# Performance work log

Hardware: AMD Instinct MI355X
Metric: run time of the kernel (lower is better)

## Reference

```python
import jax, jax.numpy as jnp
import numpy as np

K = 16          # num neighbor samples
SHARE = 8       # share_planes


def _conv1x1(x, w, b=None):
    # x: [B, Cin, N, K], w: [Cout, Cin]
    y = jnp.einsum('oc,bcnk->bonk', w, x)
    if b is not None:
        y = y + b[None, :, None, None]
    return y


def setup_inputs() -> dict:
    key = jax.random.key(0)
    ks = jax.random.split(key, 18)
    B, CIN, N = 4, 64, 16384
    MID, OUT, PT = 64, 128, 8
    s = 0.05  # weight scale

    def w(k, shape):
        return jax.random.normal(k, shape, jnp.float32) * s

    return {
        'sm_feats': jax.random.normal(ks[0], (B, CIN, N, K), jnp.float32),
        'sm_ppfs': jax.random.normal(ks[1], (B, PT, N, K), jnp.float32),
        'w0': w(ks[2], (OUT, CIN)),   'b0': w(ks[3], (OUT,)),
        'w1': w(ks[4], (MID, OUT)),   'b1': w(ks[5], (MID,)),
        'w2': w(ks[6], (MID, OUT)),   'b2': w(ks[7], (MID,)),
        'w3': w(ks[8], (MID, OUT)),   'b3': w(ks[9], (MID,)),
        'pw1': w(ks[10], (MID, PT)),
        'pw2': w(ks[11], (MID, MID)),
        'cw1': w(ks[12], (MID // SHARE, MID * K)),
        'cw2': w(ks[13], (K * MID // SHARE, MID // SHARE)), 'cb2': w(ks[14], (K * MID // SHARE,)),
        'wout': w(ks[15], (OUT, MID)), 'bout': w(ks[16], (OUT,)),
    }


def reference(sm_feats, sm_ppfs, w0, b0, w1, b1, w2, b2, w3, b3,
              pw1, pw2, cw1, cw2, cb2, wout, bout):
    B, _, N, k = sm_feats.shape
    xn = jax.nn.relu(_conv1x1(sm_feats, w0, b0))          # [B, OUT, N, K]
    x = xn[:, :, :, 0:1]                                   # [B, OUT, N, 1]
    identity = x
    x1 = _conv1x1(x, w1, b1)                               # [B, MID, N, 1]
    x2 = _conv1x1(xn, w2, b2)                              # [B, MID, N, K]
    x3 = _conv1x1(xn, w3, b3)                              # [B, MID, N, K]
    ptf = _conv1x1(jax.nn.relu(_conv1x1(sm_ppfs, pw1)), pw2)  # [B, MID, N, K]
    x3 = x3 + ptf
    xfs = x1 - x2 + ptf                                    # [B, MID, N, K]
    mid = xfs.shape[1]
    # transpose(2,3).view(B, MID*K, 1, N)
    xfs = jnp.transpose(xfs, (0, 1, 3, 2)).reshape(B, mid * k, 1, N)
    h = jax.nn.relu(_conv1x1(xfs, cw1))                    # [B, MID//S, 1, N]
    wl = _conv1x1(h, cw2, cb2)                             # [B, K*MID//S, 1, N]
    wl = wl.reshape(B, mid // SHARE, k, N)
    w = jax.nn.softmax(wl, axis=2)                         # softmax over K samples
    w = jnp.transpose(w, (0, 1, 3, 2))                     # [B, MID//S, N, K]
    w = jnp.tile(w, (1, SHARE, 1, 1))                      # [B, MID, N, K]
    out = jax.nn.relu(jnp.sum(w * x3, axis=3, keepdims=True))  # [B, MID, N, 1]
    out = _conv1x1(out, wout, bout) + identity             # [B, OUT, N, 1]
    return out[:, :, :, 0]                                 # [B, OUT, N]
```

## Files before the change

kernel.cpp:

```cpp
#include <hip/hip_runtime.h>
#include <stdint.h>

typedef unsigned int uint32;
typedef __attribute__((ext_vector_type(4))) float f32x4;
typedef __attribute__((ext_vector_type(4))) uint32 u32x4;
typedef __attribute__((ext_vector_type(8))) short bf16x8;

#define NPOS_TOTAL 65536
#define WPB 4
#define POS_PER_WAVE 16
#define NBLOCKS 1024
#define CSTRIDE 262144

#define OFF_AW0 0
#define OFF_W2N 4096
#define OFF_PW1 8192
#define N_LDS_TAB 9216
#define OFF_PW2G 9216
#define OFF_W3G 11264
#define OFF_CW1 15360
#define OFF_W1 19456
#define OFF_CW2 23552
#define OFF_WOUT 24064

__device__ __forceinline__ uint32 pack_bf16(float lo, float hi) {
  uint32 a = __builtin_bit_cast(uint32, lo);
  uint32 b = __builtin_bit_cast(uint32, hi);
  return ((b + 0x8000u) & 0xffff0000u) | ((a + 0x8000u) >> 16);
}
__device__ __forceinline__ float bf_lo(uint32 u) { return __builtin_bit_cast(float, u << 16); }
__device__ __forceinline__ float bf_hi(uint32 u) { return __builtin_bit_cast(float, u & 0xffff0000u); }
__device__ __forceinline__ float bcast(float v, int l) {
  return __builtin_bit_cast(float, __builtin_amdgcn_readlane(__builtin_bit_cast(int, v), l));
}
__device__ __forceinline__ uint32 cvt_pk(float lo, float hi) {
  uint32 r;
  asm("v_cvt_pk_bf16_f32 %0, %1, %2" : "=v"(r) : "v"(lo), "v"(hi));
  return r;
}
__device__ __forceinline__ uint32 bperm(int addr, uint32 src) {
  return (uint32)__builtin_amdgcn_ds_bpermute(addr, (int)src);
}
__device__ __forceinline__ float bpermf(int addr, float src) {
  return __builtin_bit_cast(float,
      __builtin_amdgcn_ds_bpermute(addr, __builtin_bit_cast(int, src)));
}
__device__ __forceinline__ f32x4 mfma16(u32x4 a, u32x4 b, f32x4 c) {
  return __builtin_amdgcn_mfma_f32_16x16x32_bf16(
      __builtin_bit_cast(bf16x8, a), __builtin_bit_cast(bf16x8, b), c, 0, 0, 0);
}
__device__ __forceinline__ f32x4 relu4(f32x4 v) {
  f32x4 r;
  r[0] = fmaxf(v[0], 0.f);
  r[1] = fmaxf(v[1], 0.f);
  r[2] = fmaxf(v[2], 0.f);
  r[3] = fmaxf(v[3], 0.f);
  return r;
}

__global__ void pack_weights_kernel(const float* __restrict__ w0, const float* __restrict__ w1,
                                    const float* __restrict__ w2, const float* __restrict__ w3,
                                    const float* __restrict__ pw1, const float* __restrict__ pw2,
                                    const float* __restrict__ cw1, const float* __restrict__ cw2,
                                    const float* __restrict__ wout, uint32* __restrict__ ws) {
  int t = threadIdx.x + blockIdx.x * blockDim.x;
  int stride = blockDim.x * gridDim.x;

  for (int i = t; i < 4096; i += stride) {
    int r = i & 3, l = (i >> 2) & 63, ts = i >> 8;
    int mt = ts >> 1, s = ts & 1;
    int o = mt * 16 + (l & 15);
    int c = s * 32 + ((l >> 4) << 3) + 2 * r;
    ws[OFF_AW0 + i] = pack_bf16(w0[o * 64 + c], w0[o * 64 + c + 1]);
  }
  for (int i = t; i < 4096; i += stride) {
    int r = i & 3, l = (i >> 2) & 63, ts = i >> 8;
    int nt = ts >> 2, s = ts & 3;
    int c = nt * 16 + (l & 15);
    int o = s * 32 + ((l >> 4) << 3) + 2 * r;
    ws[OFF_W2N + i] = pack_bf16(-w2[c * 128 + o], -w2[c * 128 + o + 1]);
    ws[OFF_W3G + i] = pack_bf16(w3[c * 128 + o], w3[c * 128 + o + 1]);
    ws[OFF_W1 + i] = pack_bf16(w1[c * 128 + o], w1[c * 128 + o + 1]);
  }
  for (int i = t; i < 1024; i += stride) {
    int r = i & 3, l = (i >> 2) & 63, nt = i >> 8;
    int m = nt * 16 + (l & 15);
    int qq = ((l >> 4) << 3) + 2 * r;
    float lo = (qq < 8) ? pw1[m * 8 + qq] : 0.f;
    float hi = (qq < 8) ? pw1[m * 8 + qq + 1] : 0.f;
    ws[OFF_PW1 + i] = pack_bf16(lo, hi);
  }
  for (int i = t; i < 2048; i += stride) {
    int r = i & 3, l = (i >> 2) & 63, ts = i >> 8;
    int nt = ts >> 1, s = ts & 1;
    int m2 = nt * 16 + (l & 15);
    int m = s * 32 + ((l >> 4) << 3) + 2 * r;
    ws[OFF_PW2G + i] = pack_bf16(pw2[m2 * 64 + m], pw2[m2 * 64 + m + 1]);
  }
  for (int i = t; i < 4096; i += stride) {
    int rr = i & 3, l = (i >> 2) & 63, th = i >> 8;
    int j = th >> 1, h = th & 1;
    int d = h * 4 + rr;
    int qq = l & 15, gg = l >> 4;
    int e0 = 2 * d, e1 = 2 * d + 1;
    int c0 = (e0 >> 2) * 16 + qq, k0 = gg * 4 + (e0 & 3);
    int c1 = (e1 >> 2) * 16 + qq, k1 = gg * 4 + (e1 & 3);
    ws[OFF_CW1 + i] = pack_bf16(cw1[j * 1024 + c0 * 16 + k0], cw1[j * 1024 + c1 * 16 + k1]);
  }
  for (int i = t; i < 512; i += stride) {
    int j = i >> 6, l2 = i & 63;
    ws[OFF_CW2 + i] = pack_bf16(cw2[l2 * 8 + j], cw2[(l2 + 64) * 8 + j]);
  }
  for (int i = t; i < 4096; i += stride) {
    int r = i & 3, l = (i >> 2) & 63, c4 = i >> 8;
    int c = 4 * c4 + r;
    ws[OFF_WOUT + i] = pack_bf16(wout[l * 64 + c], wout[(l + 64) * 64 + c]);
  }
}

__launch_bounds__(256, 4)
__global__ void pt_mfma(const float* __restrict__ feats, const float* __restrict__ ppfs,
                        const float* __restrict__ b0, const float* __restrict__ b1,
                        const float* __restrict__ b2, const float* __restrict__ b3,
                        const float* __restrict__ cb2, const float* __restrict__ bout,
                        const uint32* __restrict__ ws, float* __restrict__ out) {
  __shared__ uint32 sT[N_LDS_TAB];
  __shared__ float sId[WPB][128];

  const int tid = threadIdx.x;
  {
    u32x4* dst = (u32x4*)sT;
    const u32x4* src = (const u32x4*)ws;
#pragma unroll 1
    for (int i = tid; i < N_LDS_TAB / 4; i += 256) dst[i] = src[i];
  }
  __syncthreads();

  const int lane = tid & 63;
  const int wv = tid >> 6;
  const int q = lane & 15;
  const int g = lane >> 4;
  const bool isLo = (lane < 32);
  const bool qlo = ((q & 4) == 0);

  const int addrLo = 4 * (q + 16 * ((2 * g) & 3));
  const int addrHi = 4 * (q + 16 * ((2 * g + 1) & 3));
  const int addrC0 = 4 * (16 * g);
  const int addrI0 = 4 * ((q & 3) * 16 + 4 * g);

  float bfsF[4], b3F[4];
#pragma unroll
  for (int nt = 0; nt < 4; nt++) {
    bfsF[nt] = b1[nt * 16 + q] - b2[nt * 16 + q];
    b3F[nt] = b3[nt * 16 + q];
  }
  const float cb2A = cb2[lane], cb2B = cb2[lane + 64];
  const float boutA0 = bout[lane], boutB0 = bout[lane + 64];

  float* idp = &sId[wv][0];

  const int wgid = blockIdx.x * WPB + wv;
  const int p0 = wgid * POS_PER_WAVE;

  int zoff = 0;

  float oA0 = 0.f, oA1 = 0.f, oA2 = 0.f, oB0 = 0.f, oB1 = 0.f, oB2 = 0.f;

#pragma unroll 1
  for (int pi = 0; pi < POS_PER_WAVE; ++pi) {
    asm volatile("" : "+v"(zoff));
    const int p = p0 + pi;
    const int b = p >> 14, npos = p & 16383;

    const u32x4* gcw1_4 = (const u32x4*)(ws + OFF_CW1) + zoff;
    const u32x4* gw1_4 = (const u32x4*)(ws + OFF_W1) + zoff;
    const u32x4* gw3_4 = (const u32x4*)(ws + OFF_W3G) + zoff;
    const u32x4* gpw2_4 = (const u32x4*)(ws + OFF_PW2G) + zoff;
    const u32x4* gwout4 = (const u32x4*)(ws + OFF_WOUT) + zoff;
    const uint32* gcw2p = ws + OFF_CW2 + zoff;

    u32x4 fB[2];
    {
      const float* fbase = feats + (size_t)(b * 64) * CSTRIDE + npos * 16 + q;
#pragma unroll
      for (int s = 0; s < 2; s++) {
#pragma unroll
        for (int t2 = 0; t2 < 4; t2++) {
          int c0 = s * 32 + 8 * g + 2 * t2;
          float v0 = fbase[(size_t)c0 * CSTRIDE];
          float v1 = fbase[(size_t)c0 * CSTRIDE + CSTRIDE];
          fB[s][t2] = cvt_pk(v0, v1);
        }
      }
    }

    u32x4 ppA = {0u, 0u, 0u, 0u};
    if (g == 0) {
      const float* pbase = ppfs + (size_t)(b * 8) * CSTRIDE + npos * 16 + q;
      float pv[8];
#pragma unroll
      for (int j = 0; j < 8; j++) pv[j] = pbase[(size_t)j * CSTRIDE];
#pragma unroll
      for (int t2 = 0; t2 < 4; t2++) ppA[t2] = cvt_pk(pv[2 * t2], pv[2 * t2 + 1]);
    }

    f32x4 xnD[8];
#pragma unroll
    for (int mt = 0; mt < 8; mt++) {
      f32x4 acc = *(const f32x4*)(b0 + mt * 16 + 4 * g);
#pragma unroll
      for (int s = 0; s < 2; s++) {
        u32x4 aw = *(const u32x4*)&sT[OFF_AW0 + ((mt * 2 + s) * 64 + lane) * 4 + zoff];
        acc = mfma16(aw, fB[s], acc);
      }
      xnD[mt] = relu4(acc);
    }

    if (q == 0) {
#pragma unroll
      for (int mt = 0; mt < 8; mt++) *(f32x4*)(idp + mt * 16 + 4 * g) = xnD[mt];
    }

    u32x4 XNB[4];
#pragma unroll
    for (int s = 0; s < 4; s++) {
      uint32 dA0 = cvt_pk(xnD[2 * s][0], xnD[2 * s][1]);
      uint32 dA1 = cvt_pk(xnD[2 * s][2], xnD[2 * s][3]);
      uint32 dB0 = cvt_pk(xnD[2 * s + 1][0], xnD[2 * s + 1][1]);
      uint32 dB1 = cvt_pk(xnD[2 * s + 1][2], xnD[2 * s + 1][3]);
      uint32 pa, pb;
      pa = bperm(addrLo, dA0); pb = bperm(addrLo, dB0); XNB[s][0] = isLo ? pa : pb;
      pa = bperm(addrLo, dA1); pb = bperm(addrLo, dB1); XNB[s][1] = isLo ? pa : pb;
      pa = bperm(addrHi, dA0); pb = bperm(addrHi, dB0); XNB[s][2] = isLo ? pa : pb;
      pa = bperm(addrHi, dA1); pb = bperm(addrHi, dB1); XNB[s][3] = isLo ? pa : pb;
    }

    u32x4 xc0[4];
#pragma unroll
    for (int s = 0; s < 4; s++) {
#pragma unroll
      for (int r = 0; r < 4; r++) xc0[s][r] = bperm(addrC0, XNB[s][r]);
    }

    f32x4 tD[4];
#pragma unroll
    for (int nt = 0; nt < 4; nt++) {
      f32x4 z = {0.f, 0.f, 0.f, 0.f};
      u32x4 bw = *(const u32x4*)&sT[OFF_PW1 + (nt * 64 + lane) * 4 + zoff];
      tD[nt] = relu4(mfma16(ppA, bw, z));
    }
    u32x4 tA[2];
#pragma unroll
    for (int s = 0; s < 2; s++) {
      uint32 dA0 = cvt_pk(tD[2 * s][0], tD[2 * s][1]);
      uint32 dA1 = cvt_pk(tD[2 * s][2], tD[2 * s][3]);
      uint32 dB0 = cvt_pk(tD[2 * s + 1][0], tD[2 * s + 1][1]);
      uint32 dB1 = cvt_pk(tD[2 * s + 1][2], tD[2 * s + 1][3]);
      uint32 pa, pb;
      pa = bperm(addrLo, dA0); pb = bperm(addrLo, dB0); tA[s][0] = isLo ? pa : pb;
      pa = bperm(addrLo, dA1); pb = bperm(addrLo, dB1); tA[s][1] = isLo ? pa : pb;
      pa = bperm(addrHi, dA0); pb = bperm(addrHi, dB0); tA[s][2] = isLo ? pa : pb;
      pa = bperm(addrHi, dA1); pb = bperm(addrHi, dB1); tA[s][3] = isLo ? pa : pb;
    }
    f32x4 ptfD[4];
#pragma unroll
    for (int nt = 0; nt < 4; nt++) {
      f32x4 acc = {0.f, 0.f, 0.f, 0.f};
#pragma unroll
      for (int s = 0; s < 2; s++) {
        u32x4 bw = gpw2_4[(nt * 2 + s) * 64 + lane];
        acc = mfma16(tA[s], bw, acc);
      }
      ptfD[nt] = acc;
    }

    f32x4 xfs[4], x3v[4];
#pragma unroll
    for (int nt = 0; nt < 4; nt++) {
      f32x4 acc = {bfsF[nt], bfsF[nt], bfsF[nt], bfsF[nt]};
#pragma unroll
      for (int s = 0; s < 4; s++) {
        u32x4 bw = *(const u32x4*)&sT[OFF_W2N + ((nt * 4 + s) * 64 + lane) * 4 + zoff];
        acc = mfma16(XNB[s], bw, acc);
      }
#pragma unroll
      for (int s = 0; s < 4; s++) {
        u32x4 bw = gw1_4[(nt * 4 + s) * 64 + lane];
        acc = mfma16(xc0[s], bw, acc);
      }
      xfs[nt] = acc + ptfD[nt];

      f32x4 acc3 = {b3F[nt], b3F[nt], b3F[nt], b3F[nt]};
#pragma unroll
      for (int s = 0; s < 4; s++) {
        u32x4 bw = gw3_4[(nt * 4 + s) * 64 + lane];
        acc3 = mfma16(XNB[s], bw, acc3);
      }
      x3v[nt] = acc3 + ptfD[nt];
    }

    float hp[8];
#pragma unroll
    for (int j = 0; j < 8; j++) {
      float acc = 0.f;
#pragma unroll
      for (int h = 0; h < 2; h++) {
        u32x4 cwv = gcw1_4[(j * 2 + h) * 64 + lane];
#pragma unroll
        for (int rr = 0; rr < 4; rr++) {
          const int d = h * 4 + rr;
          const int nt = d >> 1;
          const int rb = (2 * d) & 3;
          acc = fmaf(bf_lo(cwv[rr]), xfs[nt][rb], acc);
          acc = fmaf(bf_hi(cwv[rr]), xfs[nt][rb + 1], acc);
        }
      }
      hp[j] = acc;
    }
#pragma unroll
    for (int j = 0; j < 8; j++) {
      float v = hp[j];
#pragma unroll
      for (int s = 1; s < 64; s <<= 1) v += __shfl_xor(v, s, 64);
      hp[j] = fmaxf(v, 0.f);
    }

    float wlA = cb2A, wlB = cb2B;
#pragma unroll
    for (int j = 0; j < 8; j++) {
      uint32 wp = gcw2p[j * 64 + lane];
      wlA = fmaf(bf_lo(wp), hp[j], wlA);
      wlB = fmaf(bf_hi(wp), hp[j], wlB);
    }

    float mA = wlA, mB = wlB;
#pragma unroll
    for (int s = 1; s < 16; s <<= 1) {
      mA = fmaxf(mA, __shfl_xor(mA, s, 64));
      mB = fmaxf(mB, __shfl_xor(mB, s, 64));
    }
    float eA = __expf(wlA - mA), eB = __expf(wlB - mB);
    float sA = eA, sB = eB;
#pragma unroll
    for (int s = 1; s < 16; s <<= 1) {
      sA += __shfl_xor(sA, s, 64);
      sB += __shfl_xor(sB, s, 64);
    }
    float smA = eA / sA, smB = eB / sB;

    float wI[4];
#pragma unroll
    for (int r = 0; r < 4; r++) {
      float wa = bpermf(addrI0 + 4 * r, smA);
      float wb = bpermf(addrI0 + 4 * r, smB);
      wI[r] = qlo ? wa : wb;
    }
    float om[4];
#pragma unroll
    for (int nt = 0; nt < 4; nt++) {
      float acc_o = 0.f;
#pragma unroll
      for (int r = 0; r < 4; r++) acc_o = fmaf(wI[r], x3v[nt][r], acc_o);
      acc_o += __shfl_xor(acc_o, 16, 64);
      acc_o += __shfl_xor(acc_o, 32, 64);
      om[nt] = fmaxf(acc_o, 0.f);
    }

    float outA = boutA0 + idp[lane];
    float outB = boutB0 + idp[lane + 64];
#pragma unroll
    for (int c4 = 0; c4 < 16; c4++) {
      u32x4 wp4 = gwout4[c4 * 64 + lane];
#pragma unroll
      for (int r = 0; r < 4; r++) {
        float sv = bcast(om[c4 >> 2], (4 * c4 + r) & 15);
        outA = fmaf(bf_lo(wp4[r]), sv, outA);
        outB = fmaf(bf_hi(wp4[r]), sv, outB);
      }
    }

    const int ph = pi & 3;
    if (ph == 0) { oA0 = outA; oB0 = outB; }
    else if (ph == 1) { oA1 = outA; oB1 = outB; }
    else if (ph == 2) { oA2 = outA; oB2 = outB; }
    else {
      f32x4 vA, vB;
      vA[0] = oA0; vA[1] = oA1; vA[2] = oA2; vA[3] = outA;
      vB[0] = oB0; vB[1] = oB1; vB[2] = oB2; vB[3] = outB;
      *(f32x4*)(out + (size_t)(b * 128 + lane) * 16384 + (npos - 3)) = vA;
      *(f32x4*)(out + (size_t)(b * 128 + lane + 64) * 16384 + (npos - 3)) = vB;
    }
  }
}

extern "C" void kernel_launch(void* const* d_in, const int* in_sizes, int n_in,
                              void* d_out, int out_size, void* d_ws, size_t ws_size,
                              hipStream_t stream) {
  const float* feats = (const float*)d_in[0];
  const float* ppfs = (const float*)d_in[1];
  const float* w0 = (const float*)d_in[2];
  const float* b0 = (const float*)d_in[3];
  const float* w1 = (const float*)d_in[4];
  const float* b1 = (const float*)d_in[5];
  const float* w2 = (const float*)d_in[6];
  const float* b2 = (const float*)d_in[7];
  const float* w3 = (const float*)d_in[8];
  const float* b3 = (const float*)d_in[9];
  const float* pw1 = (const float*)d_in[10];
  const float* pw2 = (const float*)d_in[11];
  const float* cw1 = (const float*)d_in[12];
  const float* cw2 = (const float*)d_in[13];
  const float* cb2 = (const float*)d_in[14];
  const float* wout = (const float*)d_in[15];
  const float* bout = (const float*)d_in[16];
  (void)in_sizes; (void)n_in; (void)out_size; (void)ws_size;

  uint32* ws = (uint32*)d_ws;

  hipLaunchKernelGGL(pack_weights_kernel, dim3(8), dim3(256), 0, stream,
                     w0, w1, w2, w3, pw1, pw2, cw1, cw2, wout, ws);
  hipLaunchKernelGGL(pt_mfma, dim3(NBLOCKS), dim3(256), 0, stream,
                     feats, ppfs, b0, b1, b2, b3, cb2, bout, ws, (float*)d_out);
}
```

Before: 890.8 us.

## Process two positions per loop iteration to reuse weight fragments

```diff
diff --git a/kernel.cpp b/kernel.cpp
--- a/kernel.cpp
+++ b/kernel.cpp
@@ -8,8 +8,8 @@
 
 #define NPOS_TOTAL 65536
 #define WPB 4
-#define POS_PER_WAVE 16
-#define NBLOCKS 1024
+#define POS_PER_WAVE 32
+#define NBLOCKS 512
 #define CSTRIDE 262144
 
 #define OFF_AW0 0
@@ -118,14 +118,14 @@
   }
 }
 
-__launch_bounds__(256, 4)
+__launch_bounds__(256, 2)
 __global__ void pt_mfma(const float* __restrict__ feats, const float* __restrict__ ppfs,
                         const float* __restrict__ b0, const float* __restrict__ b1,
                         const float* __restrict__ b2, const float* __restrict__ b3,
                         const float* __restrict__ cb2, const float* __restrict__ bout,
                         const uint32* __restrict__ ws, float* __restrict__ out) {
   __shared__ uint32 sT[N_LDS_TAB];
-  __shared__ float sId[WPB][128];
+  __shared__ float sId[WPB][2][128];
 
   const int tid = threadIdx.x;
   {
@@ -157,20 +157,27 @@
   const float cb2A = cb2[lane], cb2B = cb2[lane + 64];
   const float boutA0 = bout[lane], boutB0 = bout[lane + 64];
 
-  float* idp = &sId[wv][0];
+  float* idp0 = &sId[wv][0][0];
+  float* idp1 = &sId[wv][1][0];
 
   const int wgid = blockIdx.x * WPB + wv;
   const int p0 = wgid * POS_PER_WAVE;
+  const int b = p0 >> 14;
+  const int nbase = p0 & 16383;
+
+  const float* fbase = feats + (size_t)(b * 64) * CSTRIDE + nbase * 16 + q;
+  const float* pbase = ppfs + (size_t)(b * 8) * CSTRIDE + nbase * 16 + q;
+  float* outAptr = out + (size_t)(b * 128 + lane) * 16384 + nbase;
+  float* outBptr = out + (size_t)(b * 128 + lane + 64) * 16384 + nbase;
 
   int zoff = 0;
 
-  float oA0 = 0.f, oA1 = 0.f, oA2 = 0.f, oB0 = 0.f, oB1 = 0.f, oB2 = 0.f;
+  float sA0 = 0.f, sA1 = 0.f, sB0 = 0.f, sB1 = 0.f;
 
 #pragma unroll 1
-  for (int pi = 0; pi < POS_PER_WAVE; ++pi) {
+  for (int pp = 0; pp < POS_PER_WAVE / 2; ++pp) {
     asm volatile("" : "+v"(zoff));
-    const int p = p0 + pi;
-    const int b = p >> 14, npos = p & 16383;
+    const int fo = 32 * pp;
 
     const u32x4* gcw1_4 = (const u32x4*)(ws + OFF_CW1) + zoff;
     const u32x4* gw1_4 = (const u32x4*)(ws + OFF_W1) + zoff;
@@ -178,131 +185,185 @@
     const u32x4* gpw2_4 = (const u32x4*)(ws + OFF_PW2G) + zoff;
     const u32x4* gwout4 = (const u32x4*)(ws + OFF_WOUT) + zoff;
     const uint32* gcw2p = ws + OFF_CW2 + zoff;
-
-    u32x4 fB[2];
-    {
-      const float* fbase = feats + (size_t)(b * 64) * CSTRIDE + npos * 16 + q;
-#pragma unroll
-      for (int s = 0; s < 2; s++) {
-#pragma unroll
-        for (int t2 = 0; t2 < 4; t2++) {
-          int c0 = s * 32 + 8 * g + 2 * t2;
-          float v0 = fbase[(size_t)c0 * CSTRIDE];
-          float v1 = fbase[(size_t)c0 * CSTRIDE + CSTRIDE];
-          fB[s][t2] = cvt_pk(v0, v1);
-        }
-      }
-    }
-
-    u32x4 ppA = {0u, 0u, 0u, 0u};
+    const float* b0p = b0 + zoff;
+
+    u32x4 fB0[2], fB1[2];
+#pragma unroll
+    for (int s = 0; s < 2; s++) {
+#pragma unroll
+      for (int t2 = 0; t2 < 4; t2++) {
+        int c0 = s * 32 + 8 * g + 2 * t2;
+        const float* fp = fbase + (size_t)c0 * CSTRIDE + fo;
+        float v0 = fp[0];
+        float v1 = fp[CSTRIDE];
+        float w0v = fp[16];
+        float w1v = fp[CSTRIDE + 16];
+        fB0[s][t2] = cvt_pk(v0, v1);
+        fB1[s][t2] = cvt_pk(w0v, w1v);
+      }
+    }
+
+    u32x4 ppA0 = {0u, 0u, 0u, 0u}, ppA1 = {0u, 0u, 0u, 0u};
     if (g == 0) {
-      const float* pbase = ppfs + (size_t)(b * 8) * CSTRIDE + npos * 16 + q;
-      float pv[8];
-#pragma unroll
-      for (int j = 0; j < 8; j++) pv[j] = pbase[(size_t)j * CSTRIDE];
-#pragma unroll
-      for (int t2 = 0; t2 < 4; t2++) ppA[t2] = cvt_pk(pv[2 * t2], pv[2 * t2 + 1]);
-    }
-
-    f32x4 xnD[8];
+      float pv0[8], pv1[8];
+#pragma unroll
+      for (int j = 0; j < 8; j++) {
+        const float* pjp = pbase + (size_t)j * CSTRIDE + fo;
+        pv0[j] = pjp[0];
+        pv1[j] = pjp[16];
+      }
+#pragma unroll
+      for (int t2 = 0; t2 < 4; t2++) {
+        ppA0[t2] = cvt_pk(pv0[2 * t2], pv0[2 * t2 + 1]);
+        ppA1[t2] = cvt_pk(pv1[2 * t2], pv1[2 * t2 + 1]);
+      }
+    }
+
+    f32x4 xnD0[8], xnD1[8];
 #pragma unroll
     for (int mt = 0; mt < 8; mt++) {
-      f32x4 acc = *(const f32x4*)(b0 + mt * 16 + 4 * g);
+      f32x4 bb = *(const f32x4*)(b0p + mt * 16 + 4 * g);
+      f32x4 a0 = bb, a1 = bb;
 #pragma unroll
       for (int s = 0; s < 2; s++) {
         u32x4 aw = *(const u32x4*)&sT[OFF_AW0 + ((mt * 2 + s) * 64 + lane) * 4 + zoff];
-        acc = mfma16(aw, fB[s], acc);
-      }
-      xnD[mt] = relu4(acc);
+        a0 = mfma16(aw, fB0[s], a0);
+        a1 = mfma16(aw, fB1[s], a1);
+      }
+      xnD0[mt] = relu4(a0);
+      xnD1[mt] = relu4(a1);
     }
 
     if (q == 0) {
 #pragma unroll
-      for (int mt = 0; mt < 8; mt++) *(f32x4*)(idp + mt * 16 + 4 * g) = xnD[mt];
-    }
-
-    u32x4 XNB[4];
+      for (int mt = 0; mt < 8; mt++) {
+        *(f32x4*)(idp0 + mt * 16 + 4 * g) = xnD0[mt];
+        *(f32x4*)(idp1 + mt * 16 + 4 * g) = xnD1[mt];
+      }
+    }
+
+    u32x4 XNB0[4], XNB1[4];
 #pragma unroll
     for (int s = 0; s < 4; s++) {
-      uint32 dA0 = cvt_pk(xnD[2 * s][0], xnD[2 * s][1]);
-      uint32 dA1 = cvt_pk(xnD[2 * s][2], xnD[2 * s][3]);
-      uint32 dB0 = cvt_pk(xnD[2 * s + 1][0], xnD[2 * s + 1][1]);
-      uint32 dB1 = cvt_pk(xnD[2 * s + 1][2], xnD[2 * s + 1][3]);
-      uint32 pa, pb;
-      pa = bperm(addrLo, dA0); pb = bperm(addrLo, dB0); XNB[s][0] = isLo ? pa : pb;
-      pa = bperm(addrLo, dA1); pb = bperm(addrLo, dB1); XNB[s][1] = isLo ? pa : pb;
-      pa = bperm(addrHi, dA0); pb = bperm(addrHi, dB0); XNB[s][2] = isLo ? pa : pb;
-      pa = bperm(addrHi, dA1); pb = bperm(addrHi, dB1); XNB[s][3] = isLo ? pa : pb;
-    }
-
-    u32x4 xc0[4];
+      {
+        uint32 dA0 = cvt_pk(xnD0[2 * s][0], xnD0[2 * s][1]);
+        uint32 dA1 = cvt_pk(xnD0[2 * s][2], xnD0[2 * s][3]);
+        uint32 dB0 = cvt_pk(xnD0[2 * s + 1][0], xnD0[2 * s + 1][1]);
+        uint32 dB1 = cvt_pk(xnD0[2 * s + 1][2], xnD0[2 * s + 1][3]);
+        uint32 pa, pb;
+        pa = bperm(addrLo, dA0); pb = bperm(addrLo, dB0); XNB0[s][0] = isLo ? pa : pb;
+        pa = bperm(addrLo, dA1); pb = bperm(addrLo, dB1); XNB0[s][1] = isLo ? pa : pb;
+        pa = bperm(addrHi, dA0); pb = bperm(addrHi, dB0); XNB0[s][2] = isLo ? pa : pb;
+        pa = bperm(addrHi, dA1); pb = bperm(addrHi, dB1); XNB0[s][3] = isLo ? pa : pb;
+      }
+      {
+        uint32 dA0 = cvt_pk(xnD1[2 * s][0], xnD1[2 * s][1]);
+        uint32 dA1 = cvt_pk(xnD1[2 * s][2], xnD1[2 * s][3]);
+        uint32 dB0 = cvt_pk(xnD1[2 * s + 1][0], xnD1[2 * s + 1][1]);
+        uint32 dB1 = cvt_pk(xnD1[2 * s + 1][2], xnD1[2 * s + 1][3]);
+        uint32 pa, pb;
+        pa = bperm(addrLo, dA0); pb = bperm(addrLo, dB0); XNB1[s][0] = isLo ? pa : pb;
+        pa = bperm(addrLo, dA1); pb = bperm(addrLo, dB1); XNB1[s][1] = isLo ? pa : pb;
+        pa = bperm(addrHi, dA0); pb = bperm(addrHi, dB0); XNB1[s][2] = isLo ? pa : pb;
+        pa = bperm(addrHi, dA1); pb = bperm(addrHi, dB1); XNB1[s][3] = isLo ? pa : pb;
+      }
+    }
+
+    u32x4 xc0_0[4], xc0_1[4];
 #pragma unroll
     for (int s = 0; s < 4; s++) {
 #pragma unroll
-      for (int r = 0; r < 4; r++) xc0[s][r] = bperm(addrC0, XNB[s][r]);
-    }
-
-    f32x4 tD[4];
+      for (int r = 0; r < 4; r++) {
+        xc0_0[s][r] = bperm(addrC0, XNB0[s][r]);
+        xc0_1[s][r] = bperm(addrC0, XNB1[s][r]);
+      }
+    }
+
+    f32x4 tD0[4], tD1[4];
 #pragma unroll
     for (int nt = 0; nt < 4; nt++) {
       f32x4 z = {0.f, 0.f, 0.f, 0.f};
       u32x4 bw = *(const u32x4*)&sT[OFF_PW1 + (nt * 64 + lane) * 4 + zoff];
-      tD[nt] = relu4(mfma16(ppA, bw, z));
-    }
-    u32x4 tA[2];
+      tD0[nt] = relu4(mfma16(ppA0, bw, z));
+      tD1[nt] = relu4(mfma16(ppA1, bw, z));
+    }
+    u32x4 tA0[2], tA1[2];
 #pragma unroll
     for (int s = 0; s < 2; s++) {
-      uint32 dA0 = cvt_pk(tD[2 * s][0], tD[2 * s][1]);
-      uint32 dA1 = cvt_pk(tD[2 * s][2], tD[2 * s][3]);
-      uint32 dB0 = cvt_pk(tD[2 * s + 1][0], tD[2 * s + 1][1]);
-      uint32 dB1 = cvt_pk(tD[2 * s + 1][2], tD[2 * s + 1][3]);
-      uint32 pa, pb;
-      pa = bperm(addrLo, dA0); pb = bperm(addrLo, dB0); tA[s][0] = isLo ? pa : pb;
-      pa = bperm(addrLo, dA1); pb = bperm(addrLo, dB1); tA[s][1] = isLo ? pa : pb;
-      pa = bperm(addrHi, dA0); pb = bperm(addrHi, dB0); tA[s][2] = isLo ? pa : pb;
-      pa = bperm(addrHi, dA1); pb = bperm(addrHi, dB1); tA[s][3] = isLo ? pa : pb;
-    }
-    f32x4 ptfD[4];
+      {
+        uint32 dA0 = cvt_pk(tD0[2 * s][0], tD0[2 * s][1]);
+        uint32 dA1 = cvt_pk(tD0[2 * s][2], tD0[2 * s][3]);
+        uint32 dB0 = cvt_pk(tD0[2 * s + 1][0], tD0[2 * s + 1][1]);
+        uint32 dB1 = cvt_pk(tD0[2 * s + 1][2], tD0[2 * s + 1][3]);
+        uint32 pa, pb;
+        pa = bperm(addrLo, dA0); pb = bperm(addrLo, dB0); tA0[s][0] = isLo ? pa : pb;
+        pa = bperm(addrLo, dA1); pb = bperm(addrLo, dB1); tA0[s][1] = isLo ? pa : pb;
+        pa = bperm(addrHi, dA0); pb = bperm(addrHi, dB0); tA0[s][2] = isLo ? pa : pb;
+        pa = bperm(addrHi, dA1); pb = bperm(addrHi, dB1); tA0[s][3] = isLo ? pa : pb;
+      }
+      {
+        uint32 dA0 = cvt_pk(tD1[2 * s][0], tD1[2 * s][1]);
+        uint32 dA1 = cvt_pk(tD1[2 * s][2], tD1[2 * s][3]);
+        uint32 dB0 = cvt_pk(tD1[2 * s + 1][0], tD1[2 * s + 1][1]);
+        uint32 dB1 = cvt_pk(tD1[2 * s + 1][2], tD1[2 * s + 1][3]);
+        uint32 pa, pb;
+        pa = bperm(addrLo, dA0); pb = bperm(addrLo, dB0); tA1[s][0] = isLo ? pa : pb;
+        pa = bperm(addrLo, dA1); pb = bperm(addrLo, dB1); tA1[s][1] = isLo ? pa : pb;
+        pa = bperm(addrHi, dA0); pb = bperm(addrHi, dB0); tA1[s][2] = isLo ? pa : pb;
+        pa = bperm(addrHi, dA1); pb = bperm(addrHi, dB1); tA1[s][3] = isLo ? pa : pb;
+      }
+    }
+    f32x4 ptfD0[4], ptfD1[4];
 #pragma unroll
     for (int nt = 0; nt < 4; nt++) {
-      f32x4 acc = {0.f, 0.f, 0.f, 0.f};
+      f32x4 a0 = {0.f, 0.f, 0.f, 0.f};
+      f32x4 a1 = {0.f, 0.f, 0.f, 0.f};
 #pragma unroll
       for (int s = 0; s < 2; s++) {
         u32x4 bw = gpw2_4[(nt * 2 + s) * 64 + lane];
-        acc = mfma16(tA[s], bw, acc);
-      }
-      ptfD[nt] = acc;
-    }
-
-    f32x4 xfs[4], x3v[4];
+        a0 = mfma16(tA0[s], bw, a0);
+        a1 = mfma16(tA1[s], bw, a1);
+      }
+      ptfD0[nt] = a0;
+      ptfD1[nt] = a1;
+    }
+
+    f32x4 xfs0[4], xfs1[4], x3v0[4], x3v1[4];
 #pragma unroll
     for (int nt = 0; nt < 4; nt++) {
-      f32x4 acc = {bfsF[nt], bfsF[nt], bfsF[nt], bfsF[nt]};
+      f32x4 a0 = {bfsF[nt], bfsF[nt], bfsF[nt], bfsF[nt]};
+      f32x4 a1 = a0;
 #pragma unroll
       for (int s = 0; s < 4; s++) {
         u32x4 bw = *(const u32x4*)&sT[OFF_W2N + ((nt * 4 + s) * 64 + lane) * 4 + zoff];
-        acc = mfma16(XNB[s], bw, acc);
+        a0 = mfma16(XNB0[s], bw, a0);
+        a1 = mfma16(XNB1[s], bw, a1);
       }
 #pragma unroll
       for (int s = 0; s < 4; s++) {
         u32x4 bw = gw1_4[(nt * 4 + s) * 64 + lane];
-        acc = mfma16(xc0[s], bw, acc);
-      }
-      xfs[nt] = acc + ptfD[nt];
-
-      f32x4 acc3 = {b3F[nt], b3F[nt], b3F[nt], b3F[nt]};
+        a0 = mfma16(xc0_0[s], bw, a0);
+        a1 = mfma16(xc0_1[s], bw, a1);
+      }
+      xfs0[nt] = a0 + ptfD0[nt];
+      xfs1[nt] = a1 + ptfD1[nt];
+
+      f32x4 c0 = {b3F[nt], b3F[nt], b3F[nt], b3F[nt]};
+      f32x4 c1 = c0;
 #pragma unroll
       for (int s = 0; s < 4; s++) {
         u32x4 bw = gw3_4[(nt * 4 + s) * 64 + lane];
-        acc3 = mfma16(XNB[s], bw, acc3);
-      }
-      x3v[nt] = acc3 + ptfD[nt];
-    }
-
-    float hp[8];
+        c0 = mfma16(XNB0[s], bw, c0);
+        c1 = mfma16(XNB1[s], bw, c1);
+      }
+      x3v0[nt] = c0 + ptfD0[nt];
+      x3v1[nt] = c1 + ptfD1[nt];
+    }
+
+    float hp0[8], hp1[8];
 #pragma unroll
     for (int j = 0; j < 8; j++) {
-      float acc = 0.f;
+      float a0 = 0.f, a1 = 0.f;
 #pragma unroll
       for (int h = 0; h < 2; h++) {
         u32x4 cwv = gcw1_4[(j * 2 + h) * 64 + lane];
@@ -311,84 +372,115 @@
           const int d = h * 4 + rr;
           const int nt = d >> 1;
           const int rb = (2 * d) & 3;
-          acc = fmaf(bf_lo(cwv[rr]), xfs[nt][rb], acc);
-          acc = fmaf(bf_hi(cwv[rr]), xfs[nt][rb + 1], acc);
+          float wlo = bf_lo(cwv[rr]), whi = bf_hi(cwv[rr]);
+          a0 = fmaf(wlo, xfs0[nt][rb], a0);
+          a0 = fmaf(whi, xfs0[nt][rb + 1], a0);
+          a1 = fmaf(wlo, xfs1[nt][rb], a1);
+          a1 = fmaf(whi, xfs1[nt][rb + 1], a1);
         }
       }
-      hp[j] = acc;
+      hp0[j] = a0;
+      hp1[j] = a1;
     }
 #pragma unroll
     for (int j = 0; j < 8; j++) {
-      float v = hp[j];
-#pragma unroll
-      for (int s = 1; s < 64; s <<= 1) v += __shfl_xor(v, s, 64);
-      hp[j] = fmaxf(v, 0.f);
-    }
-
-    float wlA = cb2A, wlB = cb2B;
+      float v0 = hp0[j], v1 = hp1[j];
+#pragma unroll
+      for (int s = 1; s < 64; s <<= 1) {
+        v0 += __shfl_xor(v0, s, 64);
+        v1 += __shfl_xor(v1, s, 64);
+      }
+      hp0[j] = fmaxf(v0, 0.f);
+      hp1[j] = fmaxf(v1, 0.f);
+    }
+
+    float wlA0 = cb2A, wlB0 = cb2B, wlA1 = cb2A, wlB1 = cb2B;
 #pragma unroll
     for (int j = 0; j < 8; j++) {
       uint32 wp = gcw2p[j * 64 + lane];
-      wlA = fmaf(bf_lo(wp), hp[j], wlA);
-      wlB = fmaf(bf_hi(wp), hp[j], wlB);
-    }
-
-    float mA = wlA, mB = wlB;
+      float wlo = bf_lo(wp), whi = bf_hi(wp);
+      wlA0 = fmaf(wlo, hp0[j], wlA0);
+      wlB0 = fmaf(whi, hp0[j], wlB0);
+      wlA1 = fmaf(wlo, hp1[j], wlA1);
+      wlB1 = fmaf(whi, hp1[j], wlB1);
+    }
+
+    float mA0 = wlA0, mB0 = wlB0, mA1 = wlA1, mB1 = wlB1;
 #pragma unroll
     for (int s = 1; s < 16; s <<= 1) {
-      mA = fmaxf(mA, __shfl_xor(mA, s, 64));
-      mB = fmaxf(mB, __shfl_xor(mB, s, 64));
-    }
-    float eA = __expf(wlA - mA), eB = __expf(wlB - mB);
-    float sA = eA, sB = eB;
+      mA0 = fmaxf(mA0, __shfl_xor(mA0, s, 64));
+      mB0 = fmaxf(mB0, __shfl_xor(mB0, s, 64));
+      mA1 = fmaxf(mA1, __shfl_xor(mA1, s, 64));
+      mB1 = fmaxf(mB1, __shfl_xor(mB1, s, 64));
+    }
+    float eA0 = __expf(wlA0 - mA0), eB0 = __expf(wlB0 - mB0);
+    float eA1 = __expf(wlA1 - mA1), eB1 = __expf(wlB1 - mB1);
+    float sAs0 = eA0, sBs0 = eB0, sAs1 = eA1, sBs1 = eB1;
 #pragma unroll
     for (int s = 1; s < 16; s <<= 1) {
-      sA += __shfl_xor(sA, s, 64);
-      sB += __shfl_xor(sB, s, 64);
-    }
-    float smA = eA / sA, smB = eB / sB;
-
-    float wI[4];
+      sAs0 += __shfl_xor(sAs0, s, 64);
+      sBs0 += __shfl_xor(sBs0, s, 64);
+      sAs1 += __shfl_xor(sAs1, s, 64);
+      sBs1 += __shfl_xor(sBs1, s, 64);
+    }
+    float smA0 = eA0 / sAs0, smB0 = eB0 / sBs0;
+    float smA1 = eA1 / sAs1, smB1 = eB1 / sBs1;
+
+    float wI0[4], wI1[4];
 #pragma unroll
     for (int r = 0; r < 4; r++) {
-      float wa = bpermf(addrI0 + 4 * r, smA);
-      float wb = bpermf(addrI0 + 4 * r, smB);
-      wI[r] = qlo ? wa : wb;
-    }
-    float om[4];
+      float wa0 = bpermf(addrI0 + 4 * r, smA0);
+      float wb0 = bpermf(addrI0 + 4 * r, smB0);
+      float wa1 = bpermf(addrI0 + 4 * r, smA1);
+      float wb1 = bpermf(addrI0 + 4 * r, smB1);
+      wI0[r] = qlo ? wa0 : wb0;
+      wI1[r] = qlo ? wa1 : wb1;
+    }
+    float om0[4], om1[4];
 #pragma unroll
     for (int nt = 0; nt < 4; nt++) {
-      float acc_o = 0.f;
-#pragma unroll
-      for (int r = 0; r < 4; r++) acc_o = fmaf(wI[r], x3v[nt][r], acc_o);
-      acc_o += __shfl_xor(acc_o, 16, 64);
-      acc_o += __shfl_xor(acc_o, 32, 64);
-      om[nt] = fmaxf(acc_o, 0.f);
-    }
-
-    float outA = boutA0 + idp[lane];
-    float outB = boutB0 + idp[lane + 64];
+      float a0 = 0.f, a1 = 0.f;
+#pragma unroll
+      for (int r = 0; r < 4; r++) {
+        a0 = fmaf(wI0[r], x3v0[nt][r], a0);
+        a1 = fmaf(wI1[r], x3v1[nt][r], a1);
+      }
+      a0 += __shfl_xor(a0, 16, 64);
+      a0 += __shfl_xor(a0, 32, 64);
+      a1 += __shfl_xor(a1, 16, 64);
+      a1 += __shfl_xor(a1, 32, 64);
+      om0[nt] = fmaxf(a0, 0.f);
+      om1[nt] = fmaxf(a1, 0.f);
+    }
+
+    float outA_0 = boutA0 + idp0[lane];
+    float outB_0 = boutB0 + idp0[lane + 64];
+    float outA_1 = boutA0 + idp1[lane];
+    float outB_1 = boutB0 + idp1[lane + 64];
 #pragma unroll
     for (int c4 = 0; c4 < 16; c4++) {
       u32x4 wp4 = gwout4[c4 * 64 + lane];
 #pragma unroll
       for (int r = 0; r < 4; r++) {
-        float sv = bcast(om[c4 >> 2], (4 * c4 + r) & 15);
-        outA = fmaf(bf_lo(wp4[r]), sv, outA);
-        outB = fmaf(bf_hi(wp4[r]), sv, outB);
-      }
-    }
-
-    const int ph = pi & 3;
-    if (ph == 0) { oA0 = outA; oB0 = outB; }
-    else if (ph == 1) { oA1 = outA; oB1 = outB; }
-    else if (ph == 2) { oA2 = outA; oB2 = outB; }
-    else {
+        float wlo = bf_lo(wp4[r]), whi = bf_hi(wp4[r]);
+        float sv0 = bcast(om0[c4 >> 2], (4 * c4 + r) & 15);
+        float sv1 = bcast(om1[c4 >> 2], (4 * c4 + r) & 15);
+        outA_0 = fmaf(wlo, sv0, outA_0);
+        outB_0 = fmaf(whi, sv0, outB_0);
+        outA_1 = fmaf(wlo, sv1, outA_1);
+        outB_1 = fmaf(whi, sv1, outB_1);
+      }
+    }
+
+    if ((pp & 1) == 0) {
+      sA0 = outA_0; sA1 = outA_1; sB0 = outB_0; sB1 = outB_1;
+    } else {
       f32x4 vA, vB;
-      vA[0] = oA0; vA[1] = oA1; vA[2] = oA2; vA[3] = outA;
-      vB[0] = oB0; vB[1] = oB1; vB[2] = oB2; vB[3] = outB;
-      *(f32x4*)(out + (size_t)(b * 128 + lane) * 16384 + (npos - 3)) = vA;
-      *(f32x4*)(out + (size_t)(b * 128 + lane + 64) * 16384 + (npos - 3)) = vB;
+      vA[0] = sA0; vA[1] = sA1; vA[2] = outA_0; vA[3] = outA_1;
+      vB[0] = sB0; vB[1] = sB1; vB[2] = outB_0; vB[3] = outB_1;
+      const int goff = 4 * (pp >> 1);
+      *(f32x4*)(outAptr + goff) = vA;
+      *(f32x4*)(outBptr + goff) = vB;
     }
   }
 }
```

New measurement: 858.4 us. 3.6% less time.
